# Performance work log

Measured on AMD Instinct MI355X. Metric: run time of the kernel, lower is better.

## Reference

```python
import jax, jax.numpy as jnp
import numpy as np

B, S, D = 1, 4096, 2048
H, KV, HD = 16, 4, 128
GROUPS = H // KV
SCALE = HD ** -0.5
ROPE_BASE = 10000.0
NEG = -1e9


def _rope_tables():
    inv_freq = 1.0 / (ROPE_BASE ** (jnp.arange(0, HD, 2, dtype=jnp.float32) / HD))  # [HD/2]
    pos = jnp.arange(S, dtype=jnp.float32)
    freqs = pos[:, None] * inv_freq[None, :]            # [S, HD/2]
    emb = jnp.concatenate([freqs, freqs], axis=-1)      # [S, HD] (HF convention)
    return jnp.cos(emb)[None], jnp.sin(emb)[None]       # [1, S, HD]


def setup_inputs() -> dict:
    key = jax.random.key(0)
    ks = jax.random.split(key, 6)
    cos, sin = _rope_tables()
    causal = jnp.tril(jnp.ones((S, S), dtype=bool))
    attention_mask = jnp.where(causal, 0.0, NEG).astype(jnp.float32)[None, None]  # [1,1,S,S]
    std = 0.02
    return {
        "hidden_states": jax.random.normal(ks[0], (B, S, D), jnp.float32),
        "cos": cos.astype(jnp.float32),
        "sin": sin.astype(jnp.float32),
        "attention_mask": attention_mask,
        "wq": jax.random.normal(ks[1], (H * HD, D), jnp.float32) * std,
        "wk": jax.random.normal(ks[2], (KV * HD, D), jnp.float32) * std,
        "wv": jax.random.normal(ks[3], (KV * HD, D), jnp.float32) * std,
        "wo": jax.random.normal(ks[4], (D, H * HD), jnp.float32) * std,
    }


def _rotate_half(x):
    x1, x2 = x[..., : HD // 2], x[..., HD // 2:]
    return jnp.concatenate([-x2, x1], axis=-1)


def reference(hidden_states, cos, sin, attention_mask, wq, wk, wv, wo):
    b, s, _ = hidden_states.shape
    # projections -> [B, n_heads, S, HD]
    q = (hidden_states @ wq.T).reshape(b, s, H, HD).transpose(0, 2, 1, 3)
    k = (hidden_states @ wk.T).reshape(b, s, KV, HD).transpose(0, 2, 1, 3)
    v = (hidden_states @ wv.T).reshape(b, s, KV, HD).transpose(0, 2, 1, 3)
    # RoPE (HF apply_rotary_pos_emb, unsqueeze head dim)
    c, sn = cos[:, None], sin[:, None]
    q = q * c + _rotate_half(q) * sn
    k = k * c + _rotate_half(k) * sn
    # GQA: repeat kv heads
    k = jnp.repeat(k, GROUPS, axis=1)
    v = jnp.repeat(v, GROUPS, axis=1)
    # eager attention
    scores = jnp.einsum("bhqd,bhkd->bhqk", q, k) * SCALE + attention_mask
    attn = jax.nn.softmax(scores, axis=-1)
    out = jnp.einsum("bhqk,bhkd->bhqd", attn, v)
    out = out.transpose(0, 2, 1, 3).reshape(b, s, H * HD)
    # output projection (all-reduce is identity at world_size=1)
    return out @ wo.T
```

## Files before the change

kernel.cpp:

```cpp
#include <hip/hip_runtime.h>
#include <hip/hip_bf16.h>

#define SEQ   4096
#define DMODEL 2048
#define NHEAD 16
#define NKVH  4
#define HDIM  128
#define NQ    (NHEAD*HDIM)
#define NKV   (NKVH*HDIM)
#define NQKV  (NQ + 2*NKV)
#define SCALE 0.08838834764831845f
#define LOG2E 1.4426950408889634f
#define SCL2  (SCALE * LOG2E)

typedef __bf16 bf16x4 __attribute__((ext_vector_type(4)));
typedef __bf16 bf16x8 __attribute__((ext_vector_type(8)));
typedef float  f32x4  __attribute__((ext_vector_type(4)));

#define GLOBAL_CPTR(x) ((const __attribute__((address_space(1))) void*)(x))
#define LDS_PTR(x)     ((__attribute__((address_space(3))) void*)(x))

__global__ __launch_bounds__(256)
void convert_kernel(__bf16* __restrict__ dst, const float* __restrict__ src, int n8)
{
    const int i = blockIdx.x * 256 + threadIdx.x;
    if (i >= n8) return;
    const size_t e0 = (size_t)i * 8;
    const float4 a = *(const float4*)(src + e0);
    const float4 b = *(const float4*)(src + e0 + 4);
    bf16x8 o;
    o[0]=(__bf16)a.x; o[1]=(__bf16)a.y; o[2]=(__bf16)a.z; o[3]=(__bf16)a.w;
    o[4]=(__bf16)b.x; o[5]=(__bf16)b.y; o[6]=(__bf16)b.z; o[7]=(__bf16)b.w;
    *(bf16x8*)(dst + e0) = o;
}

__global__ __launch_bounds__(256)
void gemm_bt(const __bf16* __restrict__ A, const __bf16* __restrict__ Bw,
             void* __restrict__ Cv, __bf16* __restrict__ kb2, __bf16* __restrict__ vt2,
             const float* __restrict__ ct, const float* __restrict__ st,
             int M, int N, int K, int cmode)
{
    __shared__ alignas(16) __bf16 As[128*32];
    __shared__ alignas(16) __bf16 Bs[128*32];

    const int tid  = threadIdx.x;
    const int w    = tid >> 6;
    const int lane = tid & 63;
    const int l16  = lane & 15;
    const int quad = lane >> 4;
    const int m0 = blockIdx.y * 128;
    const int n0 = blockIdx.x * 128;

    const int srow = lane >> 2;
    const int scol = (lane & 3) * 8;

    const int wm = (w >> 1) * 64;
    int coff[4];
    #pragma unroll
    for (int nt = 0; nt < 4; ++nt)
        coff[nt] = (cmode == 3) ? ((w & 1) * 32 + ((nt & 2) ? 64 : 0) + (nt & 1) * 16)
                                : ((w & 1) * 64 + nt * 16);

    f32x4 acc[4][4];
    #pragma unroll
    for (int mt = 0; mt < 4; ++mt)
        #pragma unroll
        for (int nt = 0; nt < 4; ++nt)
            acc[mt][nt] = (f32x4){0.f, 0.f, 0.f, 0.f};

    for (int k0 = 0; k0 < K; k0 += 32) {
        __syncthreads();
        #pragma unroll
        for (int c = 0; c < 2; ++c) {
            const int r0 = w * 32 + c * 16;
            const __bf16* ga = A + (size_t)(m0 + r0 + srow) * K + k0 + scol;
            __builtin_amdgcn_global_load_lds(GLOBAL_CPTR(ga), LDS_PTR(&As[r0 * 32]), 16, 0, 0);
            const __bf16* gb = Bw + (size_t)(n0 + r0 + srow) * K + k0 + scol;
            __builtin_amdgcn_global_load_lds(GLOBAL_CPTR(gb), LDS_PTR(&Bs[r0 * 32]), 16, 0, 0);
        }
        __syncthreads();

        bf16x8 af[4], bf[4];
        #pragma unroll
        for (int mt = 0; mt < 4; ++mt)
            af[mt] = *(const bf16x8*)&As[(wm + mt*16 + l16) * 32 + quad * 8];
        #pragma unroll
        for (int nt = 0; nt < 4; ++nt)
            bf[nt] = *(const bf16x8*)&Bs[(coff[nt] + l16) * 32 + quad * 8];
        #pragma unroll
        for (int mt = 0; mt < 4; ++mt)
            #pragma unroll
            for (int nt = 0; nt < 4; ++nt)
                acc[mt][nt] = __builtin_amdgcn_mfma_f32_16x16x32_bf16(
                    af[mt], bf[nt], acc[mt][nt], 0, 0, 0);
    }

    if (cmode == 3) {
        if (n0 >= 2560) {
            #pragma unroll
            for (int mt = 0; mt < 4; ++mt)
                #pragma unroll
                for (int nt = 0; nt < 4; ++nt) {
                    const int col = (n0 - 2560) + coff[nt] + l16;
                    const int row = m0 + wm + mt*16 + quad*4;
                    bf16x4 pk;
                    #pragma unroll
                    for (int r = 0; r < 4; ++r) pk[r] = (__bf16)acc[mt][nt][r];
                    *(bf16x4*)&vt2[(size_t)col * M + row] = pk;
                }
        } else {
            __bf16* dst;
            int ncols, cb;
            if (n0 < 2048) { dst = (__bf16*)Cv; ncols = NQ;  cb = n0; }
            else           { dst = kb2;         ncols = NKV; cb = n0 - 2048; }
            #pragma unroll
            for (int mt = 0; mt < 4; ++mt)
                #pragma unroll
                for (int np = 0; np < 2; ++np) {
                    const int d = coff[np] + l16;
                    #pragma unroll
                    for (int r = 0; r < 4; ++r) {
                        const int s = m0 + wm + mt*16 + quad*4 + r;
                        const float c  = ct[s * HDIM + d];
                        const float sn = st[s * HDIM + d];
                        const float x1 = acc[mt][np][r];
                        const float x2 = acc[mt][np + 2][r];
                        dst[(size_t)s * ncols + cb + d]      = (__bf16)(x1 * c - x2 * sn);
                        dst[(size_t)s * ncols + cb + d + 64] = (__bf16)(x2 * c + x1 * sn);
                    }
                }
        }
    } else if (cmode == 1) {
        float* Cf = (float*)Cv;
        #pragma unroll
        for (int mt = 0; mt < 4; ++mt)
            #pragma unroll
            for (int nt = 0; nt < 4; ++nt) {
                const int row = m0 + wm + mt*16 + quad*4;
                const int col = n0 + coff[nt] + l16;
                #pragma unroll
                for (int r = 0; r < 4; ++r)
                    Cf[(size_t)(row + r) * N + col] = acc[mt][nt][r];
            }
    } else {
        __bf16* Cb = (__bf16*)Cv;
        #pragma unroll
        for (int mt = 0; mt < 4; ++mt)
            #pragma unroll
            for (int nt = 0; nt < 4; ++nt) {
                const int row = m0 + wm + mt*16 + quad*4;
                const int col = n0 + coff[nt] + l16;
                #pragma unroll
                for (int r = 0; r < 4; ++r)
                    Cb[(size_t)(row + r) * N + col] = (__bf16)acc[mt][nt][r];
            }
    }
}

__global__ __launch_bounds__(512, 4)
void attn_kernel(__bf16* __restrict__ QO, const __bf16* __restrict__ Kb,
                 const __bf16* __restrict__ Vt)
{
    __shared__ alignas(16) __bf16 Klds[2][4][64][32];
    __shared__ alignas(16) __bf16 Vlds[2][2][128][32];
    __shared__ alignas(16) __bf16 Ps[8][16][64];

    const int tid  = threadIdx.x;
    const int w    = tid >> 6;
    const int lane = tid & 63;
    const int l16  = lane & 15;
    const int quad = lane >> 4;
    const int bx = (int)blockIdx.x;
    const int h  = (int)blockIdx.y;
    const int g  = h >> 2;
    const int nbx = (int)gridDim.x;
    const int qt = (h < 8) ? (nbx - 1 - bx) : bx;
    const int m0 = qt * 128;
    const int wrow = m0 + w * 16;

    const int srow = lane >> 2;
    const int scol = (((lane & 3) ^ ((lane >> 3) & 3)) * 8);
    const int rsw  = (quad ^ ((l16 >> 1) & 3)) * 8;

    const int kcw = w & 3;
    const int hw  = w >> 2;

    bf16x8 qf[4];
    {
        const size_t qbase = (size_t)(wrow + l16) * NQ + h * HDIM;
        #pragma unroll
        for (int kc = 0; kc < 4; ++kc)
            qf[kc] = *(const bf16x8*)&QO[qbase + kc * 32 + quad * 8];
    }

    bf16x8 onesf;
    #pragma unroll
    for (int i = 0; i < 8; ++i) onesf[i] = (__bf16)1.0f;

    const __bf16* kSrc = Kb + (size_t)(hw * 32 + srow) * NKV + g * HDIM + kcw * 32 + scol;
    const __bf16* vSrc = Vt + (size_t)(g * HDIM + kcw * 32 + srow) * SEQ + hw * 32 + scol;

    auto STAGE = [&](int jj, int b) {
        const int n0g = jj * 64;
        #pragma unroll
        for (int c = 0; c < 2; ++c) {
            __builtin_amdgcn_global_load_lds(
                GLOBAL_CPTR(kSrc + (size_t)(n0g + c * 16) * NKV),
                LDS_PTR(&Klds[b][kcw][hw * 32 + c * 16][0]), 16, 0, 0);
            __builtin_amdgcn_global_load_lds(
                GLOBAL_CPTR(vSrc + (size_t)(c * 16) * SEQ + n0g),
                LDS_PTR(&Vlds[b][hw][kcw * 32 + c * 16][0]), 16, 0, 0);
        }
    };

    f32x4 lacc = (f32x4){0.f, 0.f, 0.f, 0.f};
    f32x4 oacc[8];
    #pragma unroll
    for (int t = 0; t < 8; ++t) oacc[t] = (f32x4){0.f, 0.f, 0.f, 0.f};

    const int njt = 2 * qt + 2;
    STAGE(0, 0);
    for (int j = 0; j < njt; ++j) {
        __syncthreads();
        if (j + 1 < njt) STAGE(j + 1, (j + 1) & 1);
        const int n0g = j * 64;
        if (n0g > wrow + 15) continue;
        const int b = j & 1;

        f32x4 sacc[4];
        #pragma unroll
        for (int nt = 0; nt < 4; ++nt) sacc[nt] = (f32x4){0.f, 0.f, 0.f, 0.f};
        __builtin_amdgcn_s_setprio(1);
        #pragma unroll
        for (int kc = 0; kc < 4; ++kc) {
            #pragma unroll
            for (int nt = 0; nt < 4; ++nt) {
                const bf16x8 kf = *(const bf16x8*)&Klds[b][kc][nt * 16 + l16][rsw];
                sacc[nt] = __builtin_amdgcn_mfma_f32_16x16x32_bf16(qf[kc], kf, sacc[nt], 0, 0, 0);
            }
        }
        __builtin_amdgcn_s_setprio(0);

        const bool needmask = (n0g + 64 > wrow);
        #pragma unroll
        for (int r = 0; r < 4; ++r) {
            const int qr = wrow + quad * 4 + r;
            const int prow = quad * 4 + r;
            const int pxor = (prow & 7) << 3;
            #pragma unroll
            for (int nt = 0; nt < 4; ++nt) {
                float e = exp2f(sacc[nt][r] * SCL2);
                if (needmask && (n0g + nt * 16 + l16) > qr) e = 0.f;
                Ps[w][prow][(nt * 16 + l16) ^ pxor] = (__bf16)e;
            }
        }

        bf16x8 pa[2];
        #pragma unroll
        for (int kc = 0; kc < 2; ++kc)
            pa[kc] = *(const bf16x8*)&Ps[w][l16][(kc * 32 + quad * 8) ^ ((l16 & 7) << 3)];

        __builtin_amdgcn_s_setprio(1);
        lacc = __builtin_amdgcn_mfma_f32_16x16x32_bf16(pa[0], onesf, lacc, 0, 0, 0);
        lacc = __builtin_amdgcn_mfma_f32_16x16x32_bf16(pa[1], onesf, lacc, 0, 0, 0);
        #pragma unroll
        for (int kc = 0; kc < 2; ++kc)
            #pragma unroll
            for (int t = 0; t < 8; ++t) {
                const bf16x8 vf = *(const bf16x8*)&Vlds[b][kc][t * 16 + l16][rsw];
                oacc[t] = __builtin_amdgcn_mfma_f32_16x16x32_bf16(pa[kc], vf, oacc[t], 0, 0, 0);
            }
        __builtin_amdgcn_s_setprio(0);
    }

    float rinv[4];
    #pragma unroll
    for (int r = 0; r < 4; ++r) rinv[r] = 1.f / lacc[r];
    #pragma unroll
    for (int t = 0; t < 8; ++t)
        #pragma unroll
        for (int r = 0; r < 4; ++r) {
            const int qr = wrow + quad * 4 + r;
            QO[(size_t)qr * NQ + h * HDIM + t * 16 + l16] = (__bf16)(oacc[t][r] * rinv[r]);
        }
}

extern "C" void kernel_launch(void* const* d_in, const int* in_sizes, int n_in,
                              void* d_out, int out_size, void* d_ws, size_t ws_size,
                              hipStream_t stream)
{
    const float* hidden = (const float*)d_in[0];
    const float* cosp   = (const float*)d_in[1];
    const float* sinp   = (const float*)d_in[2];
    const float* wq = (const float*)d_in[4];
    const float* wk = (const float*)d_in[5];
    const float* wv = (const float*)d_in[6];
    const float* wo = (const float*)d_in[7];

    const size_t nw_q = (size_t)NQ  * DMODEL;
    const size_t nw_k = (size_t)NKV * DMODEL;
    const size_t nq_e = (size_t)SEQ * NQ;
    const size_t nk_e = (size_t)SEQ * NKV;

    __bf16* ws     = (__bf16*)d_ws;
    __bf16* wo_b   = ws;
    __bf16* wqkv_b = wo_b + nw_q;
    __bf16* qbuf   = wqkv_b + nw_q + 2 * nw_k;
    __bf16* kbuf   = qbuf + nq_e;
    __bf16* vtb    = kbuf + nk_e;
    __bf16* hbuf   = (__bf16*)d_out;

    const dim3 blk(256);
    convert_kernel<<<dim3(nw_q / 8 / 256), blk, 0, stream>>>(wqkv_b, wq, nw_q / 8);
    convert_kernel<<<dim3(nw_k / 8 / 256), blk, 0, stream>>>(wqkv_b + nw_q, wk, nw_k / 8);
    convert_kernel<<<dim3(nw_k / 8 / 256), blk, 0, stream>>>(wqkv_b + nw_q + nw_k, wv, nw_k / 8);
    convert_kernel<<<dim3(nw_q / 8 / 256), blk, 0, stream>>>(wo_b, wo, nw_q / 8);
    convert_kernel<<<dim3(nq_e / 8 / 256), blk, 0, stream>>>(hbuf, hidden, nq_e / 8);

    gemm_bt<<<dim3(NQKV / 128, SEQ / 128), blk, 0, stream>>>(
        hbuf, wqkv_b, qbuf, kbuf, vtb, cosp, sinp, SEQ, NQKV, DMODEL, 3);

    attn_kernel<<<dim3(SEQ / 128, NHEAD), dim3(512), 0, stream>>>(qbuf, kbuf, vtb);

    gemm_bt<<<dim3(DMODEL / 128, SEQ / 128), blk, 0, stream>>>(
        qbuf, wo_b, d_out, nullptr, nullptr, nullptr, nullptr, SEQ, DMODEL, DMODEL, 1);
}
```

Before: 426.8 us.

## Switch attention to 32x32x16 MFMA with 4 waves of 32 query rows

Rewrites the attention kernel to use 32x32x16 bf16 MFMA tiles instead of 16x16x32, with 4 waves per block each owning 32 query rows (256 threads) instead of 8 waves of 16 rows. K and V LDS tiles are laid out as full-row XOR-swizzled arrays, and the P staging and row-sum accumulation are adapted to the 32x32 accumulator layout. This is meant to raise MFMA efficiency and halve K/V LDS reads per FLOP. In exchange it uses more accumulator registers per wave, runs fewer waves per block, and coarsens causal skipping to 32-row granularity.

```diff
diff --git a/kernel.cpp b/kernel.cpp
--- a/kernel.cpp
+++ b/kernel.cpp
@@ -16,6 +16,7 @@
 typedef __bf16 bf16x4 __attribute__((ext_vector_type(4)));
 typedef __bf16 bf16x8 __attribute__((ext_vector_type(8)));
 typedef float  f32x4  __attribute__((ext_vector_type(4)));
+typedef float  f32x16 __attribute__((ext_vector_type(16)));
 
 #define GLOBAL_CPTR(x) ((const __attribute__((address_space(1))) void*)(x))
 #define LDS_PTR(x)     ((__attribute__((address_space(3))) void*)(x))
@@ -157,66 +158,68 @@
     }
 }
 
-__global__ __launch_bounds__(512, 4)
+__global__ __launch_bounds__(256, 2)
 void attn_kernel(__bf16* __restrict__ QO, const __bf16* __restrict__ Kb,
                  const __bf16* __restrict__ Vt)
 {
-    __shared__ alignas(16) __bf16 Klds[2][4][64][32];
-    __shared__ alignas(16) __bf16 Vlds[2][2][128][32];
-    __shared__ alignas(16) __bf16 Ps[8][16][64];
+    __shared__ alignas(16) __bf16 Klds[2][64][128];
+    __shared__ alignas(16) __bf16 Vlds[2][128][64];
+    __shared__ alignas(16) __bf16 Ps[4][32][64];
 
     const int tid  = threadIdx.x;
     const int w    = tid >> 6;
     const int lane = tid & 63;
-    const int l16  = lane & 15;
-    const int quad = lane >> 4;
+    const int l31  = lane & 31;
+    const int h5   = lane >> 5;
     const int bx = (int)blockIdx.x;
     const int h  = (int)blockIdx.y;
     const int g  = h >> 2;
     const int nbx = (int)gridDim.x;
     const int qt = (h < 8) ? (nbx - 1 - bx) : bx;
     const int m0 = qt * 128;
-    const int wrow = m0 + w * 16;
-
-    const int srow = lane >> 2;
-    const int scol = (((lane & 3) ^ ((lane >> 3) & 3)) * 8);
-    const int rsw  = (quad ^ ((l16 >> 1) & 3)) * 8;
-
-    const int kcw = w & 3;
-    const int hw  = w >> 2;
-
-    bf16x8 qf[4];
-    {
-        const size_t qbase = (size_t)(wrow + l16) * NQ + h * HDIM;
-        #pragma unroll
-        for (int kc = 0; kc < 4; ++kc)
-            qf[kc] = *(const bf16x8*)&QO[qbase + kc * 32 + quad * 8];
-    }
-
-    bf16x8 onesf;
-    #pragma unroll
-    for (int i = 0; i < 8; ++i) onesf[i] = (__bf16)1.0f;
-
-    const __bf16* kSrc = Kb + (size_t)(hw * 32 + srow) * NKV + g * HDIM + kcw * 32 + scol;
-    const __bf16* vSrc = Vt + (size_t)(g * HDIM + kcw * 32 + srow) * SEQ + hw * 32 + scol;
+    const int wrow = m0 + w * 32;
+
+    const int kRow = w * 4 + (lane >> 4);
+    const int kslot = (lane & 15) ^ kRow;
+    const int vRow = lane >> 3;
+    const int vslot = (lane & 7) ^ vRow;
+
+    const __bf16* kSrc = Kb + (size_t)kRow * NKV + g * HDIM + kslot * 8;
+    const __bf16* vSrc = Vt + (size_t)(g * HDIM + w * 8 + vRow) * SEQ + vslot * 8;
 
     auto STAGE = [&](int jj, int b) {
         const int n0g = jj * 64;
         #pragma unroll
-        for (int c = 0; c < 2; ++c) {
+        for (int i = 0; i < 4; ++i) {
             __builtin_amdgcn_global_load_lds(
-                GLOBAL_CPTR(kSrc + (size_t)(n0g + c * 16) * NKV),
-                LDS_PTR(&Klds[b][kcw][hw * 32 + c * 16][0]), 16, 0, 0);
+                GLOBAL_CPTR(kSrc + (size_t)(n0g + i * 16) * NKV),
+                LDS_PTR(&Klds[b][i * 16 + w * 4][0]), 16, 0, 0);
             __builtin_amdgcn_global_load_lds(
-                GLOBAL_CPTR(vSrc + (size_t)(c * 16) * SEQ + n0g),
-                LDS_PTR(&Vlds[b][hw][kcw * 32 + c * 16][0]), 16, 0, 0);
+                GLOBAL_CPTR(vSrc + (size_t)(i * 32) * SEQ + n0g),
+                LDS_PTR(&Vlds[b][i * 32 + w * 8][0]), 16, 0, 0);
         }
     };
 
-    f32x4 lacc = (f32x4){0.f, 0.f, 0.f, 0.f};
-    f32x4 oacc[8];
-    #pragma unroll
-    for (int t = 0; t < 8; ++t) oacc[t] = (f32x4){0.f, 0.f, 0.f, 0.f};
+    bf16x8 qf[8];
+    {
+        const size_t qbase = (size_t)(wrow + l31) * NQ + h * HDIM + h5 * 8;
+        #pragma unroll
+        for (int kc = 0; kc < 8; ++kc)
+            qf[kc] = *(const bf16x8*)&QO[qbase + kc * 16];
+    }
+
+    bf16x8 onesf;
+    #pragma unroll
+    for (int i = 0; i < 8; ++i) onesf[i] = (__bf16)1.0f;
+
+    f32x16 lacc;
+    f32x16 oacc[4];
+    #pragma unroll
+    for (int i = 0; i < 16; ++i) lacc[i] = 0.f;
+    #pragma unroll
+    for (int t = 0; t < 4; ++t)
+        #pragma unroll
+        for (int i = 0; i < 16; ++i) oacc[t][i] = 0.f;
 
     const int njt = 2 * qt + 2;
     STAGE(0, 0);
@@ -224,64 +227,72 @@
         __syncthreads();
         if (j + 1 < njt) STAGE(j + 1, (j + 1) & 1);
         const int n0g = j * 64;
-        if (n0g > wrow + 15) continue;
+        if (n0g > wrow + 31) continue;
         const int b = j & 1;
 
-        f32x4 sacc[4];
-        #pragma unroll
-        for (int nt = 0; nt < 4; ++nt) sacc[nt] = (f32x4){0.f, 0.f, 0.f, 0.f};
+        f32x16 sacc[2];
+        #pragma unroll
+        for (int nt = 0; nt < 2; ++nt)
+            #pragma unroll
+            for (int i = 0; i < 16; ++i) sacc[nt][i] = 0.f;
         __builtin_amdgcn_s_setprio(1);
         #pragma unroll
-        for (int kc = 0; kc < 4; ++kc) {
-            #pragma unroll
-            for (int nt = 0; nt < 4; ++nt) {
-                const bf16x8 kf = *(const bf16x8*)&Klds[b][kc][nt * 16 + l16][rsw];
-                sacc[nt] = __builtin_amdgcn_mfma_f32_16x16x32_bf16(qf[kc], kf, sacc[nt], 0, 0, 0);
+        for (int kc = 0; kc < 8; ++kc) {
+            #pragma unroll
+            for (int nt = 0; nt < 2; ++nt) {
+                const bf16x8 kf = *(const bf16x8*)
+                    &Klds[b][nt * 32 + l31][((kc * 2 + h5) ^ (lane & 15)) * 8];
+                sacc[nt] = __builtin_amdgcn_mfma_f32_32x32x16_bf16(qf[kc], kf, sacc[nt], 0, 0, 0);
             }
         }
         __builtin_amdgcn_s_setprio(0);
 
         const bool needmask = (n0g + 64 > wrow);
         #pragma unroll
-        for (int r = 0; r < 4; ++r) {
-            const int qr = wrow + quad * 4 + r;
-            const int prow = quad * 4 + r;
-            const int pxor = (prow & 7) << 3;
-            #pragma unroll
-            for (int nt = 0; nt < 4; ++nt) {
-                float e = exp2f(sacc[nt][r] * SCL2);
-                if (needmask && (n0g + nt * 16 + l16) > qr) e = 0.f;
-                Ps[w][prow][(nt * 16 + l16) ^ pxor] = (__bf16)e;
-            }
-        }
-
-        bf16x8 pa[2];
-        #pragma unroll
-        for (int kc = 0; kc < 2; ++kc)
-            pa[kc] = *(const bf16x8*)&Ps[w][l16][(kc * 32 + quad * 8) ^ ((l16 & 7) << 3)];
+        for (int nt = 0; nt < 2; ++nt) {
+            const int keyl = nt * 32 + l31;
+            const int keyg = n0g + keyl;
+            const int pcol = ((keyl >> 3) ^ 0) * 0;
+            #pragma unroll
+            for (int reg = 0; reg < 16; ++reg) {
+                const int rloc = (reg & 3) + 8 * (reg >> 2) + 4 * h5;
+                float e = exp2f(sacc[nt][reg] * SCL2);
+                if (needmask && keyg > wrow + rloc) e = 0.f;
+                Ps[w][rloc][(((keyl >> 3) ^ (rloc & 7)) << 3) + (keyl & 7)] = (__bf16)e;
+            }
+            (void)pcol;
+        }
+
+        bf16x8 pa[4];
+        #pragma unroll
+        for (int kv = 0; kv < 4; ++kv)
+            pa[kv] = *(const bf16x8*)&Ps[w][l31][((kv * 2 + h5) ^ (lane & 7)) * 8];
 
         __builtin_amdgcn_s_setprio(1);
-        lacc = __builtin_amdgcn_mfma_f32_16x16x32_bf16(pa[0], onesf, lacc, 0, 0, 0);
-        lacc = __builtin_amdgcn_mfma_f32_16x16x32_bf16(pa[1], onesf, lacc, 0, 0, 0);
-        #pragma unroll
-        for (int kc = 0; kc < 2; ++kc)
-            #pragma unroll
-            for (int t = 0; t < 8; ++t) {
-                const bf16x8 vf = *(const bf16x8*)&Vlds[b][kc][t * 16 + l16][rsw];
-                oacc[t] = __builtin_amdgcn_mfma_f32_16x16x32_bf16(pa[kc], vf, oacc[t], 0, 0, 0);
+        #pragma unroll
+        for (int kv = 0; kv < 4; ++kv)
+            lacc = __builtin_amdgcn_mfma_f32_32x32x16_bf16(pa[kv], onesf, lacc, 0, 0, 0);
+        #pragma unroll
+        for (int kv = 0; kv < 4; ++kv)
+            #pragma unroll
+            for (int ot = 0; ot < 4; ++ot) {
+                const bf16x8 vf = *(const bf16x8*)
+                    &Vlds[b][ot * 32 + l31][((kv * 2 + h5) ^ (lane & 7)) * 8];
+                oacc[ot] = __builtin_amdgcn_mfma_f32_32x32x16_bf16(pa[kv], vf, oacc[ot], 0, 0, 0);
             }
         __builtin_amdgcn_s_setprio(0);
     }
 
-    float rinv[4];
-    #pragma unroll
-    for (int r = 0; r < 4; ++r) rinv[r] = 1.f / lacc[r];
-    #pragma unroll
-    for (int t = 0; t < 8; ++t)
-        #pragma unroll
-        for (int r = 0; r < 4; ++r) {
-            const int qr = wrow + quad * 4 + r;
-            QO[(size_t)qr * NQ + h * HDIM + t * 16 + l16] = (__bf16)(oacc[t][r] * rinv[r]);
+    float rinv[16];
+    #pragma unroll
+    for (int reg = 0; reg < 16; ++reg) rinv[reg] = 1.f / lacc[reg];
+    #pragma unroll
+    for (int ot = 0; ot < 4; ++ot)
+        #pragma unroll
+        for (int reg = 0; reg < 16; ++reg) {
+            const int rloc = (reg & 3) + 8 * (reg >> 2) + 4 * h5;
+            QO[(size_t)(wrow + rloc) * NQ + h * HDIM + ot * 32 + l31] =
+                (__bf16)(oacc[ot][reg] * rinv[reg]);
         }
 }
 
@@ -320,7 +331,7 @@
     gemm_bt<<<dim3(NQKV / 128, SEQ / 128), blk, 0, stream>>>(
         hbuf, wqkv_b, qbuf, kbuf, vtb, cosp, sinp, SEQ, NQKV, DMODEL, 3);
 
-    attn_kernel<<<dim3(SEQ / 128, NHEAD), dim3(512), 0, stream>>>(qbuf, kbuf, vtb);
+    attn_kernel<<<dim3(SEQ / 128, NHEAD), dim3(256), 0, stream>>>(qbuf, kbuf, vtb);
 
     gemm_bt<<<dim3(DMODEL / 128, SEQ / 128), blk, 0, stream>>>(
         qbuf, wo_b, d_out, nullptr, nullptr, nullptr, nullptr, SEQ, DMODEL, DMODEL, 1);
```

After: 464.6 us. 1.09x slower.
